# Optimization experiments

Hardware: AMD Instinct MI355X
Metric: run time of the kernel (lower is better)

The kernel has to match this reference:

```python
import jax, jax.numpy as jnp
import numpy as np

B, S, W, D, T = 64, 512, 384, 768, 21


def setup_inputs() -> dict:
    key = jax.random.key(0)
    ks = jax.random.split(key, 8)
    hidden_states = jax.random.normal(ks[0], (B, S, D), dtype=jnp.float32)  # BERT last_hidden_state
    word_maps = jnp.sort(jax.random.randint(ks[1], (B, W), 0, S), axis=1)  # first-subword index per word
    tags = jax.random.randint(ks[2], (B, W), 0, T)
    word_mask = jnp.ones((B, W), dtype=bool)  # torchcrf requires mask[:,0] all on
    W_tag = jax.random.normal(ks[3], (T, D), dtype=jnp.float32) * 0.02  # hidden2tag weight
    b_tag = jnp.zeros((T,), dtype=jnp.float32)
    start_trans = jax.random.uniform(ks[4], (T,), minval=-0.1, maxval=0.1)
    end_trans = jax.random.uniform(ks[5], (T,), minval=-0.1, maxval=0.1)
    trans = jax.random.uniform(ks[6], (T, T), minval=-0.1, maxval=0.1)
    return dict(hidden_states=hidden_states, W_tag=W_tag, b_tag=b_tag,
                start_trans=start_trans, end_trans=end_trans, trans=trans,
                word_maps=word_maps, tags=tags, word_mask=word_mask)


def reference(hidden_states, W_tag, b_tag, start_trans, end_trans, trans,
              word_maps, tags, word_mask):
    # --- ragged subword -> word gather (vectorized form of the python loop) ---
    word_feats = jnp.take_along_axis(hidden_states, word_maps[:, :, None], axis=1)  # [B,W,D]
    # dropout is identity in eval / deterministic reference
    emissions = jnp.einsum('bwd,td->bwt', word_feats, W_tag) + b_tag  # [B,W,T]

    maskf = word_mask.astype(emissions.dtype)
    bidx = jnp.arange(tags.shape[0])

    # --- CRF numerator: score of the given tag sequence ---
    emit_sc = jnp.take_along_axis(emissions, tags[:, :, None], axis=2)[..., 0]  # [B,W]
    trans_sc = trans[tags[:, :-1], tags[:, 1:]]                                  # [B,W-1]
    num = start_trans[tags[:, 0]] + emit_sc[:, 0]
    num = num + jnp.sum((trans_sc + emit_sc[:, 1:]) * maskf[:, 1:], axis=1)
    lengths = word_mask.sum(axis=1)
    last_tags = jnp.take_along_axis(tags, (lengths - 1)[:, None], axis=1)[:, 0]
    num = num + end_trans[last_tags]

    # --- CRF denominator: log partition via forward recurrence (scan over time) ---
    def step(score, xm):
        em_t, m_t = xm  # [B,T], [B]
        nxt = jax.nn.logsumexp(score[:, :, None] + trans[None, :, :] + em_t[:, None, :], axis=1)
        return jnp.where(m_t[:, None], nxt, score), None

    score0 = start_trans[None, :] + emissions[:, 0]  # [B,T]
    score, _ = jax.lax.scan(step, score0,
                            (jnp.swapaxes(emissions[:, 1:], 0, 1), word_mask[:, 1:].T))
    log_z = jax.nn.logsumexp(score + end_trans[None, :], axis=1)  # [B]

    llh = num - log_z
    return -jnp.mean(llh)  # reduction='mean', negated
```

## Files before the change

kernel.cpp:

```cpp
#include <hip/hip_runtime.h>
#include <math.h>

#define BB 64
#define SS 512
#define WW 384
#define DD 768
#define TT 21
#define ROWS (BB*WW)
#define EMSTRIDE (WW*TT)
#define NCH 16
#define CLEN 24
#define PSTRIDE 24
#define PMATSZ (TT*PSTRIDE)
#define LN32 3.4657359027997265f
#define BKS 776

typedef short   bf16x8 __attribute__((ext_vector_type(8)));
typedef float   f32x4  __attribute__((ext_vector_type(4)));
union FragU { bf16x8 v; unsigned u[4]; };

__device__ __forceinline__ unsigned pack_bf16(unsigned lo, unsigned hi) {
    return __builtin_amdgcn_perm(hi, lo, 0x07060302);
}

__global__ __launch_bounds__(256) void emissions_kernel(
    const float* __restrict__ hidden, const int* __restrict__ word_maps,
    const float* __restrict__ W_tag, const float* __restrict__ b_tag,
    float* __restrict__ em, float* __restrict__ out)
{
    __shared__ __align__(16) unsigned short Bl[32 * BKS];
    __shared__ int rowoff[64];

    const int tid = threadIdx.x;
    const int rowBase = blockIdx.x * 64;

    if (blockIdx.x == 0 && tid == 0) out[0] = 0.0f;

    if (tid < 64) {
        int row = rowBase + tid;
        int b = row / WW;
        int w = row - b * WW;
        rowoff[tid] = b * SS + word_maps[b * WW + w];
    }

    for (int i = tid; i < TT * (DD / 4); i += 256) {
        int t = i / (DD / 4), q = i - t * (DD / 4);
        float4 wv = *(const float4*)&W_tag[t * DD + q * 4];
        *(unsigned*)&Bl[t * BKS + q * 4]     = pack_bf16(__float_as_uint(wv.x), __float_as_uint(wv.y));
        *(unsigned*)&Bl[t * BKS + q * 4 + 2] = pack_bf16(__float_as_uint(wv.z), __float_as_uint(wv.w));
    }
    __syncthreads();

    const int wv_  = tid >> 6;
    const int lane = tid & 63;
    const int l16  = lane & 15;
    const int quad = lane >> 4;

    const float* abase = hidden + (size_t)rowoff[wv_ * 16 + l16] * DD + quad * 8;
    const unsigned short* bb0 = &Bl[(     l16) * BKS + quad * 8];
    const unsigned short* bb1 = &Bl[(16 + l16) * BKS + quad * 8];

    f32x4 acc0 = {}, acc1 = {};

    float4 A0[4], A1[4];
    #pragma unroll
    for (int p = 0; p < 4; ++p) {
        A0[p] = *(const float4*)(abase + p * 32);
        A1[p] = *(const float4*)(abase + p * 32 + 4);
    }
    bf16x8 b0c = *(const bf16x8*)bb0;
    bf16x8 b1c = *(const bf16x8*)bb1;

    #pragma unroll
    for (int ks = 0; ks < DD / 32; ++ks) {
        bf16x8 b0n = b0c, b1n = b1c;
        if (ks < DD / 32 - 1) {
            b0n = *(const bf16x8*)(bb0 + (ks + 1) * 32);
            b1n = *(const bf16x8*)(bb1 + (ks + 1) * 32);
        }
        FragU a;
        a.u[0] = pack_bf16(__float_as_uint(A0[ks & 3].x), __float_as_uint(A0[ks & 3].y));
        a.u[1] = pack_bf16(__float_as_uint(A0[ks & 3].z), __float_as_uint(A0[ks & 3].w));
        a.u[2] = pack_bf16(__float_as_uint(A1[ks & 3].x), __float_as_uint(A1[ks & 3].y));
        a.u[3] = pack_bf16(__float_as_uint(A1[ks & 3].z), __float_as_uint(A1[ks & 3].w));
        if (ks < DD / 32 - 4) {
            A0[ks & 3] = *(const float4*)(abase + (ks + 4) * 32);
            A1[ks & 3] = *(const float4*)(abase + (ks + 4) * 32 + 4);
        }
        acc0 = __builtin_amdgcn_mfma_f32_16x16x32_bf16(a.v, b0c, acc0, 0, 0, 0);
        acc1 = __builtin_amdgcn_mfma_f32_16x16x32_bf16(a.v, b1c, acc1, 0, 0, 0);
        b0c = b0n; b1c = b1n;
    }

    {
        int col = l16;
        float bt = b_tag[col];
        int rbase = rowBase + wv_ * 16 + quad * 4;
        #pragma unroll
        for (int r = 0; r < 4; ++r)
            em[(size_t)(rbase + r) * TT + col] = acc0[r] + bt;
    }
    if (16 + l16 < TT) {
        int col = 16 + l16;
        float bt = b_tag[col];
        int rbase = rowBase + wv_ * 16 + quad * 4;
        #pragma unroll
        for (int r = 0; r < 4; ++r)
            em[(size_t)(rbase + r) * TT + col] = acc1[r] + bt;
    }
}

__global__ __launch_bounds__(256) void chunk_kernel(
    const float* __restrict__ em, const float* __restrict__ trans,
    float* __restrict__ Pmat)
{
    __shared__ __align__(16) float Pbuf[4][2][PMATSZ];
    __shared__ __align__(16) float gem[4][CLEN * PSTRIDE];

    const int wid  = threadIdx.x >> 6;
    const int lane = threadIdx.x & 63;
    const int id   = blockIdx.x * 4 + wid;
    const int b    = id >> 4;
    const int c    = id & (NCH - 1);
    const int s0   = 1 + c * CLEN;
    const int n    = (c == NCH - 1) ? (WW - s0) : CLEN;

    int i3r = lane / 6;
    const int jg  = lane - i3r * 6;
    const bool active = (i3r < 7) && (jg < 6);
    const int i3 = (i3r < 7) ? i3r : 6;
    const int jbase = (jg < 6 ? jg : 5) * 4;

    float4 etr[CLEN];
    #pragma unroll
    for (int k = 0; k < CLEN; ++k) {
        float4 e = make_float4(0.f, 0.f, 0.f, 0.f);
        if (k < TT) {
            e.x = (jbase + 0 < TT) ? __expf(trans[k * TT + jbase + 0]) * 0.03125f : 0.f;
            e.y = (jbase + 1 < TT) ? __expf(trans[k * TT + jbase + 1]) * 0.03125f : 0.f;
            e.z = (jbase + 2 < TT) ? __expf(trans[k * TT + jbase + 2]) * 0.03125f : 0.f;
            e.w = (jbase + 3 < TT) ? __expf(trans[k * TT + jbase + 3]) * 0.03125f : 0.f;
        }
        etr[k] = e;
    }

    for (int idx = lane; idx < n * PSTRIDE; idx += 64) {
        int tt = idx / PSTRIDE, j = idx - tt * PSTRIDE;
        float g = 1.0f;
        if (j < TT) g = __expf(em[((size_t)b * WW + (s0 + tt)) * TT + j]);
        gem[wid][idx] = g;
    }

    {
        float4 g = *(const float4*)&gem[wid][0 * PSTRIDE + jbase];
        #pragma unroll
        for (int r = 0; r < 3; ++r) {
            int i = i3 * 3 + r;
            float4 e = etr[i];
            float4 v = make_float4(e.x * g.x, e.y * g.y, e.z * g.z, e.w * g.w);
            if (active) *(float4*)&Pbuf[wid][0][i * PSTRIDE + jbase] = v;
        }
    }
    __syncthreads();

    int pp = 0;
    for (int tt = 1; tt < n; ++tt) {
        float acc[3][4];
        #pragma unroll
        for (int r = 0; r < 3; ++r)
            #pragma unroll
            for (int q = 0; q < 4; ++q) acc[r][q] = 0.f;

        const float* Pc = &Pbuf[wid][pp][0];
        #pragma unroll
        for (int kb = 0; kb < 6; ++kb) {
            float4 p0 = *(const float4*)&Pc[(i3 * 3 + 0) * PSTRIDE + kb * 4];
            float4 p1 = *(const float4*)&Pc[(i3 * 3 + 1) * PSTRIDE + kb * 4];
            float4 p2 = *(const float4*)&Pc[(i3 * 3 + 2) * PSTRIDE + kb * 4];
            #pragma unroll
            for (int kk = 0; kk < 4; ++kk) {
                float4 e = etr[kb * 4 + kk];
                float a = (kk == 0) ? p0.x : (kk == 1) ? p0.y : (kk == 2) ? p0.z : p0.w;
                float bv= (kk == 0) ? p1.x : (kk == 1) ? p1.y : (kk == 2) ? p1.z : p1.w;
                float cv= (kk == 0) ? p2.x : (kk == 1) ? p2.y : (kk == 2) ? p2.z : p2.w;
                acc[0][0] = fmaf(a, e.x, acc[0][0]); acc[0][1] = fmaf(a, e.y, acc[0][1]);
                acc[0][2] = fmaf(a, e.z, acc[0][2]); acc[0][3] = fmaf(a, e.w, acc[0][3]);
                acc[1][0] = fmaf(bv, e.x, acc[1][0]); acc[1][1] = fmaf(bv, e.y, acc[1][1]);
                acc[1][2] = fmaf(bv, e.z, acc[1][2]); acc[1][3] = fmaf(bv, e.w, acc[1][3]);
                acc[2][0] = fmaf(cv, e.x, acc[2][0]); acc[2][1] = fmaf(cv, e.y, acc[2][1]);
                acc[2][2] = fmaf(cv, e.z, acc[2][2]); acc[2][3] = fmaf(cv, e.w, acc[2][3]);
            }
        }
        float4 g = *(const float4*)&gem[wid][tt * PSTRIDE + jbase];
        if (active) {
            #pragma unroll
            for (int r = 0; r < 3; ++r) {
                float4 v = make_float4(acc[r][0] * g.x, acc[r][1] * g.y,
                                       acc[r][2] * g.z, acc[r][3] * g.w);
                *(float4*)&Pbuf[wid][1 - pp][(i3 * 3 + r) * PSTRIDE + jbase] = v;
            }
        }
        pp ^= 1;
    }

    float* dst = Pmat + (size_t)id * PMATSZ;
    for (int idx = lane; idx < PMATSZ; idx += 64)
        dst[idx] = Pbuf[wid][pp][idx];
}

__device__ __forceinline__ float lane_bcast(float v, int l) {
    return __uint_as_float(__builtin_amdgcn_readlane(__float_as_uint(v), l));
}

__global__ __launch_bounds__(64) void combine_kernel(
    const float* __restrict__ Pmat, const float* __restrict__ em,
    const int* __restrict__ tags, const float* __restrict__ start_trans,
    const float* __restrict__ end_trans, const float* __restrict__ trans,
    float* __restrict__ out)
{
    const int b = blockIdx.x;
    const int j = threadIdx.x;
    const bool act = (j < TT);
    const int jc = act ? j : (TT - 1);
    const float* emb = em + (size_t)b * EMSTRIDE;

    float s0v = start_trans[jc] + emb[jc];
    float M = act ? s0v : -1e30f;
    #pragma unroll
    for (int o = 32; o > 0; o >>= 1) M = fmaxf(M, __shfl_xor(M, o));
    float sig = act ? __expf(s0v - M) : 0.0f;

    for (int c = 0; c < NCH; ++c) {
        const float* P = Pmat + (size_t)(b * NCH + c) * PMATSZ;
        float col[TT];
        #pragma unroll
        for (int i = 0; i < TT; ++i) col[i] = P[i * PSTRIDE + jc];
        float a0 = 0.f, a1 = 0.f, a2 = 0.f;
        #pragma unroll
        for (int i = 0; i < TT; i += 3) {
            a0 = fmaf(lane_bcast(sig, i    ), col[i    ], a0);
            a1 = fmaf(lane_bcast(sig, i + 1), col[i + 1], a1);
            a2 = fmaf(lane_bcast(sig, i + 2), col[i + 2], a2);
        }
        float v = act ? (a0 + a1 + a2) : 0.0f;
        float m = v;
        #pragma unroll
        for (int o = 32; o > 0; o >>= 1) m = fmaxf(m, __shfl_xor(m, o));
        int nst = (c == NCH - 1) ? (WW - (1 + c * CLEN)) : CLEN;
        M += __logf(m) + (float)nst * LN32;
        sig = v / m;
    }

    float fin = (act && sig > 0.f) ? (M + __logf(sig) + end_trans[jc]) : -1e30f;
    float mm = fin;
    #pragma unroll
    for (int o = 32; o > 0; o >>= 1) mm = fmaxf(mm, __shfl_xor(mm, o));
    float pe = __expf(fin - mm);
    float ssum = pe;
    #pragma unroll
    for (int o = 32; o > 0; o >>= 1) ssum += __shfl_xor(ssum, o);
    float lz = mm + __logf(ssum);

    const int* tb = tags + b * WW;
    float part = 0.f;
    for (int w = j; w < WW; w += 64) {
        int tw = tb[w];
        float e = emb[w * TT + tw];
        float tsc = (w == 0) ? start_trans[tw] : trans[tb[w - 1] * TT + tw];
        part += tsc + e;
    }
    #pragma unroll
    for (int o = 32; o > 0; o >>= 1) part += __shfl_xor(part, o);

    if (j == 0) {
        float num = part + end_trans[tb[WW - 1]];
        atomicAdd(out, -(num - lz) * (1.0f / BB));
    }
}

extern "C" void kernel_launch(void* const* d_in, const int* in_sizes, int n_in,
                              void* d_out, int out_size, void* d_ws, size_t ws_size,
                              hipStream_t stream) {
    const float* hidden      = (const float*)d_in[0];
    const float* W_tag       = (const float*)d_in[1];
    const float* b_tag       = (const float*)d_in[2];
    const float* start_trans = (const float*)d_in[3];
    const float* end_trans   = (const float*)d_in[4];
    const float* trans       = (const float*)d_in[5];
    const int*   word_maps   = (const int*)  d_in[6];
    const int*   tags        = (const int*)  d_in[7];

    float* out  = (float*)d_out;
    float* em   = (float*)d_ws;
    float* Pmat = (float*)d_ws + (size_t)ROWS * TT;

    emissions_kernel<<<ROWS / 64, 256, 0, stream>>>(hidden, word_maps, W_tag, b_tag, em, out);
    chunk_kernel<<<BB * NCH / 4, 256, 0, stream>>>(em, trans, Pmat);
    combine_kernel<<<BB, 64, 0, stream>>>(Pmat, em, tags, start_trans, end_trans, trans, out);
}
```

Measured before the change: 207.8 us.

## Split emissions GEMM K dimension across wave pairs with fragment-ordered LDS weights

Each block now handles 32 rows instead of 64, with two waves per 16-row tile each covering half of D. The halves are combined through a shared-memory reduction. W_tag is stored in LDS in MFMA fragment order so each lane reads its B fragment contiguously. The aim is more blocks and shorter per-wave dependency chains to hide the latency of the gather loads. The cost is that each block repeats the W_tag conversion for half as many rows, plus an extra barrier and reduction.

```diff
diff --git a/kernel.cpp b/kernel.cpp
--- a/kernel.cpp
+++ b/kernel.cpp
@@ -13,7 +13,6 @@
 #define PSTRIDE 24
 #define PMATSZ (TT*PSTRIDE)
 #define LN32 3.4657359027997265f
-#define BKS 776
 
 typedef short   bf16x8 __attribute__((ext_vector_type(8)));
 typedef float   f32x4  __attribute__((ext_vector_type(4)));
@@ -28,15 +27,16 @@
     const float* __restrict__ W_tag, const float* __restrict__ b_tag,
     float* __restrict__ em, float* __restrict__ out)
 {
-    __shared__ __align__(16) unsigned short Bl[32 * BKS];
-    __shared__ int rowoff[64];
+    __shared__ __align__(16) unsigned short Bs[24 * 2 * 4 * 16 * 8];
+    __shared__ __align__(16) float Sred[2][64][8];
+    __shared__ int rowoff[32];
 
     const int tid = threadIdx.x;
-    const int rowBase = blockIdx.x * 64;
+    const int rowBase = blockIdx.x * 32;
 
     if (blockIdx.x == 0 && tid == 0) out[0] = 0.0f;
 
-    if (tid < 64) {
+    if (tid < 32) {
         int row = rowBase + tid;
         int b = row / WW;
         int w = row - b * WW;
@@ -45,20 +45,26 @@
 
     for (int i = tid; i < TT * (DD / 4); i += 256) {
         int t = i / (DD / 4), q = i - t * (DD / 4);
-        float4 wv = *(const float4*)&W_tag[t * DD + q * 4];
-        *(unsigned*)&Bl[t * BKS + q * 4]     = pack_bf16(__float_as_uint(wv.x), __float_as_uint(wv.y));
-        *(unsigned*)&Bl[t * BKS + q * 4 + 2] = pack_bf16(__float_as_uint(wv.z), __float_as_uint(wv.w));
+        int k  = q * 4;
+        int ks = k >> 5, quad = (k >> 3) & 3, e = k & 7;
+        int nt = t >> 4, l16 = t & 15;
+        float4 wv = *(const float4*)&W_tag[t * DD + k];
+        int off = ((ks * 2 + nt) * 4 + quad) * 128 + l16 * 8 + e;
+        *(unsigned*)&Bs[off]     = pack_bf16(__float_as_uint(wv.x), __float_as_uint(wv.y));
+        *(unsigned*)&Bs[off + 2] = pack_bf16(__float_as_uint(wv.z), __float_as_uint(wv.w));
     }
     __syncthreads();
 
     const int wv_  = tid >> 6;
+    const int rt   = wv_ >> 1;
+    const int h    = wv_ & 1;
     const int lane = tid & 63;
     const int l16  = lane & 15;
     const int quad = lane >> 4;
 
-    const float* abase = hidden + (size_t)rowoff[wv_ * 16 + l16] * DD + quad * 8;
-    const unsigned short* bb0 = &Bl[(     l16) * BKS + quad * 8];
-    const unsigned short* bb1 = &Bl[(16 + l16) * BKS + quad * 8];
+    const float* abase = hidden + (size_t)rowoff[rt * 16 + l16] * DD
+                                + h * (DD / 2) + quad * 8;
+    const unsigned short* bbase = Bs + quad * 128 + l16 * 8 + h * 12 * 1024;
 
     f32x4 acc0 = {}, acc1 = {};
 
@@ -68,22 +74,22 @@
         A0[p] = *(const float4*)(abase + p * 32);
         A1[p] = *(const float4*)(abase + p * 32 + 4);
     }
-    bf16x8 b0c = *(const bf16x8*)bb0;
-    bf16x8 b1c = *(const bf16x8*)bb1;
-
-    #pragma unroll
-    for (int ks = 0; ks < DD / 32; ++ks) {
+    bf16x8 b0c = *(const bf16x8*)(bbase);
+    bf16x8 b1c = *(const bf16x8*)(bbase + 512);
+
+    #pragma unroll
+    for (int ks = 0; ks < 12; ++ks) {
         bf16x8 b0n = b0c, b1n = b1c;
-        if (ks < DD / 32 - 1) {
-            b0n = *(const bf16x8*)(bb0 + (ks + 1) * 32);
-            b1n = *(const bf16x8*)(bb1 + (ks + 1) * 32);
+        if (ks < 11) {
+            b0n = *(const bf16x8*)(bbase + (ks + 1) * 1024);
+            b1n = *(const bf16x8*)(bbase + (ks + 1) * 1024 + 512);
         }
         FragU a;
         a.u[0] = pack_bf16(__float_as_uint(A0[ks & 3].x), __float_as_uint(A0[ks & 3].y));
         a.u[1] = pack_bf16(__float_as_uint(A0[ks & 3].z), __float_as_uint(A0[ks & 3].w));
         a.u[2] = pack_bf16(__float_as_uint(A1[ks & 3].x), __float_as_uint(A1[ks & 3].y));
         a.u[3] = pack_bf16(__float_as_uint(A1[ks & 3].z), __float_as_uint(A1[ks & 3].w));
-        if (ks < DD / 32 - 4) {
+        if (ks < 8) {
             A0[ks & 3] = *(const float4*)(abase + (ks + 4) * 32);
             A1[ks & 3] = *(const float4*)(abase + (ks + 4) * 32 + 4);
         }
@@ -92,21 +98,34 @@
         b0c = b0n; b1c = b1n;
     }
 
-    {
-        int col = l16;
-        float bt = b_tag[col];
-        int rbase = rowBase + wv_ * 16 + quad * 4;
-        #pragma unroll
-        for (int r = 0; r < 4; ++r)
-            em[(size_t)(rbase + r) * TT + col] = acc0[r] + bt;
-    }
-    if (16 + l16 < TT) {
-        int col = 16 + l16;
-        float bt = b_tag[col];
-        int rbase = rowBase + wv_ * 16 + quad * 4;
-        #pragma unroll
-        for (int r = 0; r < 4; ++r)
-            em[(size_t)(rbase + r) * TT + col] = acc1[r] + bt;
+    if (h == 1) {
+        #pragma unroll
+        for (int r = 0; r < 4; ++r) {
+            Sred[rt][lane][r]     = acc0[r];
+            Sred[rt][lane][r + 4] = acc1[r];
+        }
+    }
+    __syncthreads();
+
+    if (h == 0) {
+        #pragma unroll
+        for (int r = 0; r < 4; ++r) {
+            acc0[r] += Sred[rt][lane][r];
+            acc1[r] += Sred[rt][lane][r + 4];
+        }
+        int rbase = rowBase + rt * 16 + quad * 4;
+        {
+            float bt = b_tag[l16];
+            #pragma unroll
+            for (int r = 0; r < 4; ++r)
+                em[(size_t)(rbase + r) * TT + l16] = acc0[r] + bt;
+        }
+        if (16 + l16 < TT) {
+            float bt = b_tag[16 + l16];
+            #pragma unroll
+            for (int r = 0; r < 4; ++r)
+                em[(size_t)(rbase + r) * TT + 16 + l16] = acc1[r] + bt;
+        }
     }
 }
 
@@ -294,7 +313,7 @@
     float* em   = (float*)d_ws;
     float* Pmat = (float*)d_ws + (size_t)ROWS * TT;
 
-    emissions_kernel<<<ROWS / 64, 256, 0, stream>>>(hidden, word_maps, W_tag, b_tag, em, out);
+    emissions_kernel<<<ROWS / 32, 256, 0, stream>>>(hidden, word_maps, W_tag, b_tag, em, out);
     chunk_kernel<<<BB * NCH / 4, 256, 0, stream>>>(em, trans, Pmat);
     combine_kernel<<<BB, 64, 0, stream>>>(Pmat, em, tags, start_trans, end_trans, trans, out);
 }
```

Result: no change. 206.4 us (median of 2 runs) (-0.7%).
